# Kernel optimization log

Measured on AMD Instinct MI355X. Metric: run time of the kernel, lower is better.

## Reference

```python
import jax, jax.numpy as jnp
import numpy as np

N = 100000   # nodes in batched graph
E = 1600000  # edges (before self-loops)
D = 128      # in_dim == hidden_dim == num_outputs
G = 64       # graphs in the batch


def setup_inputs() -> dict:
    key = jax.random.key(0)
    ks = jax.random.split(key, 8)
    s = 1.0 / np.sqrt(D)
    x = jax.random.normal(ks[0], (N, D), jnp.float32)
    src = jax.random.randint(ks[1], (E,), 0, N, dtype=jnp.int64)
    dst = jax.random.randint(ks[2], (E,), 0, N, dtype=jnp.int64)
    graph_ids = jnp.sort(jax.random.randint(ks[3], (N,), 0, G, dtype=jnp.int64))
    W0 = jax.random.normal(ks[4], (D, D), jnp.float32) * s
    W1 = jax.random.normal(ks[5], (D, D), jnp.float32) * s
    W2 = jax.random.normal(ks[6], (D, D), jnp.float32) * s
    b0 = jnp.zeros((D,), jnp.float32)
    b1 = jnp.zeros((D,), jnp.float32)
    b2 = jnp.zeros((D,), jnp.float32)
    return {"x": x, "W0": W0, "b0": b0, "W1": W1, "b1": b1,
            "W2": W2, "b2": b2, "src": src, "dst": dst, "graph_ids": graph_ids}


def reference(x, W0, b0, W1, b1, W2, b2, src, dst, graph_ids):
    n = x.shape[0]
    loops = jnp.arange(n, dtype=src.dtype)
    src_f = jnp.concatenate([src, loops])  # add self-loops once (dgl.add_self_loop)
    dst_f = jnp.concatenate([dst, loops])
    ones_e = jnp.ones(src_f.shape, x.dtype)
    deg_out = jax.ops.segment_sum(ones_e, src_f, num_segments=n)  # >=1 (self-loop)
    deg_in = jax.ops.segment_sum(ones_e, dst_f, num_segments=n)
    cs = jax.lax.rsqrt(deg_out)[:, None]  # source norm (GraphConv norm='both')
    cd = jax.lax.rsqrt(deg_in)[:, None]   # destination norm

    def gcn_layer(h, W, b):
        m = (h * cs)[src_f]                                   # [E+N, D] gather
        agg = jax.ops.segment_sum(m, dst_f, num_segments=n)   # scatter-add SpMM
        return jax.nn.relu((agg * cd) @ W + b)                # F.relu(conv(g, h))

    h = gcn_layer(x, W0, b0)
    h = gcn_layer(h, W1, b1)
    h = gcn_layer(h, W2, b2)

    # dgl.mean_nodes: per-graph mean over nodes
    sums = jax.ops.segment_sum(h, graph_ids, num_segments=G)
    cnt = jax.ops.segment_sum(jnp.ones((n, 1), h.dtype), graph_ids, num_segments=G)
    return sums / jnp.maximum(cnt, 1.0)  # [G, D] logits
```

## Files before the change

### kernel.cpp

```cpp
#include <hip/hip_runtime.h>
#include <stdint.h>

#define D 128
#define CAP 64
#define HB 128
#define CH 50000

typedef __attribute__((ext_vector_type(8))) short bf16x8;
typedef __attribute__((ext_vector_type(4))) float f32x4;

__device__ inline unsigned short f2bf(float x) {
  union { float f; uint32_t u; } v; v.f = x;
  uint32_t u = v.u;
  u += 0x7fffu + ((u >> 16) & 1u);
  return (unsigned short)(u >> 16);
}
__device__ inline float bflo(uint32_t u) {
  union { uint32_t u; float f; } v; v.u = u << 16; return v.f;
}
__device__ inline float bfhi(uint32_t u) {
  union { uint32_t u; float f; } v; v.u = u & 0xffff0000u; return v.f;
}
__device__ inline uint32_t packbf(float lo, float hi) {
  return (uint32_t)f2bf(lo) | ((uint32_t)f2bf(hi) << 16);
}

__global__ __launch_bounds__(256) void hist_kernel(
    const int* __restrict__ src, const int* __restrict__ dst,
    unsigned int* __restrict__ parts_s, unsigned int* __restrict__ parts_d,
    int E, int N) {
  __shared__ unsigned int lbs[CH / 8];
  __shared__ unsigned int lbd[CH / 8];
  int b = blockIdx.x & (HB - 1);
  int lo = (blockIdx.x >> 7) * CH;
  for (int i = threadIdx.x; i < CH / 8; i += 256) { lbs[i] = 0; lbd[i] = 0; }
  __syncthreads();
  int per = (E + HB - 1) / HB;
  int e0 = b * per;
  int e1 = min(e0 + per, E);
  for (int e = e0 + threadIdx.x; e < e1; e += 256) {
    int rs = src[e] - lo;
    if ((unsigned)rs < CH) atomicAdd(&lbs[rs >> 3], 1u << ((rs & 7) * 4));
    int rd = dst[e] - lo;
    if ((unsigned)rd < CH) atomicAdd(&lbd[rd >> 3], 1u << ((rd & 7) * 4));
  }
  __syncthreads();
  int nu = (N + 7) / 8;
  int base = lo >> 3;
  int cu = min(CH / 8, nu - base);
  unsigned int* ps = parts_s + (size_t)b * nu + base;
  unsigned int* pd = parts_d + (size_t)b * nu + base;
  for (int i = threadIdx.x; i < cu; i += 256) { ps[i] = lbs[i]; pd[i] = lbd[i]; }
}

__global__ void scan_norm_kernel(const unsigned char* __restrict__ parts_s,
                                 const unsigned char* __restrict__ parts_d,
                                 unsigned char* __restrict__ offs_d,
                                 int* __restrict__ degd,
                                 float* __restrict__ cs, float* __restrict__ cd, int N) {
  int t = blockIdx.x * blockDim.x + threadIdx.x;
  int i0 = t * 2;
  if (i0 >= N) return;
  int nb = N / 2;
  int ds0 = 0, ds1 = 0, dd0 = 0, dd1 = 0;
  for (int b = 0; b < HB; b++) {
    unsigned char sv = parts_s[(size_t)b * nb + t];
    ds0 += sv & 15; ds1 += sv >> 4;
    unsigned char dv = parts_d[(size_t)b * nb + t];
    offs_d[(size_t)b * N + i0]     = (unsigned char)min(dd0, 255);
    offs_d[(size_t)b * N + i0 + 1] = (unsigned char)min(dd1, 255);
    dd0 += dv & 15; dd1 += dv >> 4;
  }
  degd[i0] = dd0;     degd[i0 + 1] = dd1;
  cs[i0] = rsqrtf((float)ds0 + 1.0f);
  cs[i0 + 1] = rsqrtf((float)ds1 + 1.0f);
  cd[i0] = rsqrtf((float)dd0 + 1.0f);
  cd[i0 + 1] = rsqrtf((float)dd1 + 1.0f);
}

__global__ __launch_bounds__(256) void fill_kernel(
    const int* __restrict__ src, const int* __restrict__ dst,
    const unsigned char* __restrict__ offs_d, int* __restrict__ col, int E, int N) {
  __shared__ unsigned int lcur[CH / 8];
  int b = blockIdx.x & (HB - 1);
  int lo = (blockIdx.x >> 7) * CH;
  for (int i = threadIdx.x; i < CH / 8; i += 256) lcur[i] = 0;
  __syncthreads();
  int per = (E + HB - 1) / HB;
  int e0 = b * per;
  int e1 = min(e0 + per, E);
  const unsigned char* offb = offs_d + (size_t)b * N;
  for (int e = e0 + threadIdx.x; e < e1; e += 256) {
    int d = dst[e];
    int rd = d - lo;
    if ((unsigned)rd < CH) {
      unsigned old = atomicAdd(&lcur[rd >> 3], 1u << ((rd & 7) * 4));
      int local = (old >> ((rd & 7) * 4)) & 0xF;
      int pos = (int)offb[d] + local;
      if (pos < CAP) col[(size_t)d * CAP + pos] = src[e];
    }
  }
}

__global__ void prep_kernel(const float* __restrict__ W0, const float* __restrict__ W1,
                            const float* __restrict__ W2, unsigned short* __restrict__ Wt,
                            const float* __restrict__ x, const float* __restrict__ cs,
                            uint32_t* __restrict__ xs, int total2,
                            float* __restrict__ cnt, int G,
                            float* __restrict__ outz, int out_total) {
  int i = blockIdx.x * blockDim.x + threadIdx.x;
  if (i < 3 * 16384) {
    int l = i >> 14, r = i & 16383;
    int n = r >> 7, k = r & 127;
    const float* W = (l == 0) ? W0 : (l == 1) ? W1 : W2;
    Wt[i] = f2bf(W[k * 128 + n]);
  }
  if (i < G) cnt[i] = 0.f;
  if (i < out_total) outz[i] = 0.f;
  if (i < total2) {
    float2 v = ((const float2*)x)[i];
    float c = cs[i >> 6];
    xs[i] = packbf(v.x * c, v.y * c);
  }
}

__global__ __launch_bounds__(512) void fused_layer_kernel(
    const uint32_t* __restrict__ hin, const unsigned short* __restrict__ Wt,
    const float* __restrict__ bias, const float* __restrict__ cd,
    const float* __restrict__ rowscale, const int* __restrict__ degd,
    const int* __restrict__ col, unsigned short* __restrict__ hout, int N) {
  __shared__ __align__(16) uint32_t At[16 * 68];

  int wv = threadIdx.x >> 6;
  int lane = threadIdx.x & 63;
  int m = lane & 15;
  int quad = lane >> 4;

  bf16x8 bfr[4];
#pragma unroll
  for (int c = 0; c < 4; c++)
    bfr[c] = *(const bf16x8*)(Wt + (size_t)(16 * wv + m) * 128 + c * 32 + quad * 8);

#pragma unroll
  for (int j = 0; j < 2; j++) {
    int w = __builtin_amdgcn_readfirstlane(blockIdx.x * 16 + wv * 2 + j);
    float accx = 0.f, accy = 0.f;
    if (w < N) {
      int n = min(degd[w], CAP);
      const int* cw = col + (size_t)w * CAP;
      const uint32_t* hl = hin + lane;
      uint32_t selfv = hl[(size_t)w * 64];
      accx = bflo(selfv); accy = bfhi(selfv);
      int i = 0;
      for (; i + 7 < n; i += 8) {
        int s0 = cw[i],     s1 = cw[i + 1], s2 = cw[i + 2], s3 = cw[i + 3];
        int s4 = cw[i + 4], s5 = cw[i + 5], s6 = cw[i + 6], s7 = cw[i + 7];
        uint32_t v0 = hl[(size_t)s0 * 64];
        uint32_t v1 = hl[(size_t)s1 * 64];
        uint32_t v2 = hl[(size_t)s2 * 64];
        uint32_t v3 = hl[(size_t)s3 * 64];
        uint32_t v4 = hl[(size_t)s4 * 64];
        uint32_t v5 = hl[(size_t)s5 * 64];
        uint32_t v6 = hl[(size_t)s6 * 64];
        uint32_t v7 = hl[(size_t)s7 * 64];
        accx += bflo(v0); accy += bfhi(v0);
        accx += bflo(v1); accy += bfhi(v1);
        accx += bflo(v2); accy += bfhi(v2);
        accx += bflo(v3); accy += bfhi(v3);
        accx += bflo(v4); accy += bfhi(v4);
        accx += bflo(v5); accy += bfhi(v5);
        accx += bflo(v6); accy += bfhi(v6);
        accx += bflo(v7); accy += bfhi(v7);
      }
      for (; i + 3 < n; i += 4) {
        int s0 = cw[i], s1 = cw[i + 1], s2 = cw[i + 2], s3 = cw[i + 3];
        uint32_t v0 = hl[(size_t)s0 * 64];
        uint32_t v1 = hl[(size_t)s1 * 64];
        uint32_t v2 = hl[(size_t)s2 * 64];
        uint32_t v3 = hl[(size_t)s3 * 64];
        accx += bflo(v0); accy += bfhi(v0);
        accx += bflo(v1); accy += bfhi(v1);
        accx += bflo(v2); accy += bfhi(v2);
        accx += bflo(v3); accy += bfhi(v3);
      }
      for (; i < n; i++) {
        uint32_t v = hl[(size_t)cw[i] * 64];
        accx += bflo(v); accy += bfhi(v);
      }
      float cdv = cd[w];
      accx *= cdv; accy *= cdv;
    }
    At[(wv * 2 + j) * 68 + lane] = packbf(accx, accy);
  }
  __syncthreads();

  const unsigned short* arow = (const unsigned short*)At + m * 136;
  f32x4 acc = f32x4{0.f, 0.f, 0.f, 0.f};
#pragma unroll
  for (int c = 0; c < 4; c++) {
    bf16x8 a = *(const bf16x8*)(arow + c * 32 + quad * 8);
    acc = __builtin_amdgcn_mfma_f32_16x16x32_bf16(a, bfr[c], acc, 0, 0, 0);
  }
  int colb = 16 * wv + m;
  float bv = bias[colb];
#pragma unroll
  for (int i = 0; i < 4; i++) {
    int r = blockIdx.x * 16 + quad * 4 + i;
    if (r < N) {
      float v = acc[i] + bv;
      v = v > 0.f ? v : 0.f;
      if (rowscale) v *= rowscale[r];
      hout[(size_t)r * D + colb] = f2bf(v);
    }
  }
}

__global__ void pool_kernel(const unsigned short* __restrict__ h, const int* __restrict__ gid,
                            float* __restrict__ outsum, float* __restrict__ cnt, int N) {
  int v0 = blockIdx.x * 64;
  if (v0 >= N) return;
  int d = threadIdx.x;
  int vend = min(v0 + 64, N);
  int cur = gid[v0];
  float acc = 0.f, c = 0.f;
  for (int v = v0; v < vend; v++) {
    int g = gid[v];
    if (g != cur) {
      atomicAdd(&outsum[cur * D + d], acc);
      if (d == 0) atomicAdd(&cnt[cur], c);
      acc = 0.f; c = 0.f; cur = g;
    }
    unsigned short hv = __builtin_nontemporal_load(&h[(size_t)v * D + d]);
    union { uint32_t u; float f; } cv; cv.u = (uint32_t)hv << 16;
    acc += cv.f;
    c += 1.f;
  }
  atomicAdd(&outsum[cur * D + d], acc);
  if (d == 0) atomicAdd(&cnt[cur], c);
}

__global__ void div_kernel(float* out, const float* __restrict__ cnt, int total) {
  int i = blockIdx.x * blockDim.x + threadIdx.x;
  if (i < total) out[i] /= fmaxf(cnt[i >> 7], 1.0f);
}

extern "C" void kernel_launch(void* const* d_in, const int* in_sizes, int n_in,
                              void* d_out, int out_size, void* d_ws, size_t ws_size,
                              hipStream_t stream) {
  const float* x  = (const float*)d_in[0];
  const float* W0 = (const float*)d_in[1];
  const float* b0 = (const float*)d_in[2];
  const float* W1 = (const float*)d_in[3];
  const float* b1 = (const float*)d_in[4];
  const float* W2 = (const float*)d_in[5];
  const float* b2 = (const float*)d_in[6];
  const int* src  = (const int*)d_in[7];
  const int* dst  = (const int*)d_in[8];
  const int* gid  = (const int*)d_in[9];

  const int N = in_sizes[0] / D;
  const int E = in_sizes[7];
  const int G = out_size / D;
  const int nu = (N + 7) / 8;

  uint32_t* hsA = (uint32_t*)d_ws;
  uint32_t* hsB = hsA + (size_t)N * 64;
  int* col      = (int*)(hsB + (size_t)N * 64);
  int* degd     = col + (size_t)N * CAP;
  float* csb    = (float*)(degd + N);
  float* cdb    = csb + N;
  float* cnt    = cdb + N;
  unsigned short* Wt = (unsigned short*)(cnt + G);
  unsigned int* parts_s = (unsigned int*)(Wt + 3 * 16384);
  unsigned int* parts_d = parts_s + (size_t)HB * nu;
  unsigned char* offs_d = (unsigned char*)(parts_d + (size_t)HB * nu);

  const int nch = (N + CH - 1) / CH;
  hist_kernel<<<HB * nch, 256, 0, stream>>>(src, dst, parts_s, parts_d, E, N);
  scan_norm_kernel<<<(N / 2 + 255) / 256, 256, 0, stream>>>(
      (const unsigned char*)parts_s, (const unsigned char*)parts_d, offs_d,
      degd, csb, cdb, N);
  fill_kernel<<<HB * nch, 256, 0, stream>>>(src, dst, offs_d, col, E, N);
  prep_kernel<<<(N * 64 + 255) / 256, 256, 0, stream>>>(
      W0, W1, W2, Wt, x, csb, hsA, N * 64, cnt, G, (float*)d_out, out_size);

  const int ltiles = (N + 15) / 16;

  fused_layer_kernel<<<ltiles, 512, 0, stream>>>(hsA, Wt, b0, cdb, csb, degd, col,
                                                 (unsigned short*)hsB, N);
  fused_layer_kernel<<<ltiles, 512, 0, stream>>>(hsB, Wt + 16384, b1, cdb, csb, degd, col,
                                                 (unsigned short*)hsA, N);
  fused_layer_kernel<<<ltiles, 512, 0, stream>>>(hsA, Wt + 2 * 16384, b2, cdb, nullptr, degd, col,
                                                 (unsigned short*)hsB, N);

  pool_kernel<<<(N + 63) / 64, 128, 0, stream>>>((const unsigned short*)hsB, gid,
                                                 (float*)d_out, cnt, N);
  div_kernel<<<(out_size + 255) / 256, 256, 0, stream>>>((float*)d_out, cnt, out_size);
}
```

Baseline: 460.6 us.

## Fold prep work into hist/fill kernels, halve chunk size, use 4-wave layer blocks

Result: slower. 473.1 us (+2.7%).

```diff
diff --git a/kernel.cpp b/kernel.cpp
--- a/kernel.cpp
+++ b/kernel.cpp
@@ -4,7 +4,7 @@
 #define D 128
 #define CAP 64
 #define HB 128
-#define CH 50000
+#define CH 25000
 
 typedef __attribute__((ext_vector_type(8))) short bf16x8;
 typedef __attribute__((ext_vector_type(4))) float f32x4;
@@ -28,7 +28,10 @@
 __global__ __launch_bounds__(256) void hist_kernel(
     const int* __restrict__ src, const int* __restrict__ dst,
     unsigned int* __restrict__ parts_s, unsigned int* __restrict__ parts_d,
-    int E, int N) {
+    int E, int N,
+    const float* __restrict__ W0, const float* __restrict__ W1,
+    const float* __restrict__ W2, unsigned short* __restrict__ Wt,
+    float* __restrict__ cnt, int G, float* __restrict__ outz, int out_total) {
   __shared__ unsigned int lbs[CH / 8];
   __shared__ unsigned int lbd[CH / 8];
   int b = blockIdx.x & (HB - 1);
@@ -51,6 +54,16 @@
   unsigned int* ps = parts_s + (size_t)b * nu + base;
   unsigned int* pd = parts_d + (size_t)b * nu + base;
   for (int i = threadIdx.x; i < cu; i += 256) { ps[i] = lbs[i]; pd[i] = lbd[i]; }
+
+  int gs = gridDim.x * 256;
+  for (int i = blockIdx.x * 256 + threadIdx.x; i < 3 * 16384; i += gs) {
+    int l = i >> 14, r = i & 16383;
+    int n = r >> 7, k = r & 127;
+    const float* W = (l == 0) ? W0 : (l == 1) ? W1 : W2;
+    Wt[i] = f2bf(W[k * 128 + n]);
+  }
+  for (int i = blockIdx.x * 256 + threadIdx.x; i < G; i += gs) cnt[i] = 0.f;
+  for (int i = blockIdx.x * 256 + threadIdx.x; i < out_total; i += gs) outz[i] = 0.f;
 }
 
 __global__ void scan_norm_kernel(const unsigned char* __restrict__ parts_s,
@@ -80,7 +93,9 @@
 
 __global__ __launch_bounds__(256) void fill_kernel(
     const int* __restrict__ src, const int* __restrict__ dst,
-    const unsigned char* __restrict__ offs_d, int* __restrict__ col, int E, int N) {
+    const unsigned char* __restrict__ offs_d, int* __restrict__ col, int E, int N,
+    const float* __restrict__ x, const float* __restrict__ cs,
+    uint32_t* __restrict__ xs) {
   __shared__ unsigned int lcur[CH / 8];
   int b = blockIdx.x & (HB - 1);
   int lo = (blockIdx.x >> 7) * CH;
@@ -100,31 +115,16 @@
       if (pos < CAP) col[(size_t)d * CAP + pos] = src[e];
     }
   }
-}
-
-__global__ void prep_kernel(const float* __restrict__ W0, const float* __restrict__ W1,
-                            const float* __restrict__ W2, unsigned short* __restrict__ Wt,
-                            const float* __restrict__ x, const float* __restrict__ cs,
-                            uint32_t* __restrict__ xs, int total2,
-                            float* __restrict__ cnt, int G,
-                            float* __restrict__ outz, int out_total) {
-  int i = blockIdx.x * blockDim.x + threadIdx.x;
-  if (i < 3 * 16384) {
-    int l = i >> 14, r = i & 16383;
-    int n = r >> 7, k = r & 127;
-    const float* W = (l == 0) ? W0 : (l == 1) ? W1 : W2;
-    Wt[i] = f2bf(W[k * 128 + n]);
-  }
-  if (i < G) cnt[i] = 0.f;
-  if (i < out_total) outz[i] = 0.f;
-  if (i < total2) {
+  int total2 = N * 64;
+  int gs = gridDim.x * 256;
+  for (int i = blockIdx.x * 256 + threadIdx.x; i < total2; i += gs) {
     float2 v = ((const float2*)x)[i];
     float c = cs[i >> 6];
     xs[i] = packbf(v.x * c, v.y * c);
   }
 }
 
-__global__ __launch_bounds__(512) void fused_layer_kernel(
+__global__ __launch_bounds__(256) void fused_layer_kernel(
     const uint32_t* __restrict__ hin, const unsigned short* __restrict__ Wt,
     const float* __restrict__ bias, const float* __restrict__ cd,
     const float* __restrict__ rowscale, const int* __restrict__ degd,
@@ -136,14 +136,17 @@
   int m = lane & 15;
   int quad = lane >> 4;
 
-  bf16x8 bfr[4];
-#pragma unroll
-  for (int c = 0; c < 4; c++)
-    bfr[c] = *(const bf16x8*)(Wt + (size_t)(16 * wv + m) * 128 + c * 32 + quad * 8);
-
-#pragma unroll
-  for (int j = 0; j < 2; j++) {
-    int w = __builtin_amdgcn_readfirstlane(blockIdx.x * 16 + wv * 2 + j);
+  bf16x8 bfr[2][4];
+#pragma unroll
+  for (int tt = 0; tt < 2; tt++) {
+    int tile = 2 * wv + tt;
+#pragma unroll
+    for (int c = 0; c < 4; c++)
+      bfr[tt][c] = *(const bf16x8*)(Wt + (size_t)(16 * tile + m) * 128 + c * 32 + quad * 8);
+  }
+
+  for (int j = 0; j < 4; j++) {
+    int w = __builtin_amdgcn_readfirstlane(blockIdx.x * 16 + wv * 4 + j);
     float accx = 0.f, accy = 0.f;
     if (w < N) {
       int n = min(degd[w], CAP);
@@ -190,27 +193,32 @@
       float cdv = cd[w];
       accx *= cdv; accy *= cdv;
     }
-    At[(wv * 2 + j) * 68 + lane] = packbf(accx, accy);
+    At[(wv * 4 + j) * 68 + lane] = packbf(accx, accy);
   }
   __syncthreads();
 
   const unsigned short* arow = (const unsigned short*)At + m * 136;
-  f32x4 acc = f32x4{0.f, 0.f, 0.f, 0.f};
-#pragma unroll
-  for (int c = 0; c < 4; c++) {
-    bf16x8 a = *(const bf16x8*)(arow + c * 32 + quad * 8);
-    acc = __builtin_amdgcn_mfma_f32_16x16x32_bf16(a, bfr[c], acc, 0, 0, 0);
-  }
-  int colb = 16 * wv + m;
-  float bv = bias[colb];
-#pragma unroll
-  for (int i = 0; i < 4; i++) {
-    int r = blockIdx.x * 16 + quad * 4 + i;
-    if (r < N) {
-      float v = acc[i] + bv;
-      v = v > 0.f ? v : 0.f;
-      if (rowscale) v *= rowscale[r];
-      hout[(size_t)r * D + colb] = f2bf(v);
+  bf16x8 afrag[4];
+#pragma unroll
+  for (int c = 0; c < 4; c++) afrag[c] = *(const bf16x8*)(arow + c * 32 + quad * 8);
+
+#pragma unroll
+  for (int tt = 0; tt < 2; tt++) {
+    f32x4 acc = f32x4{0.f, 0.f, 0.f, 0.f};
+#pragma unroll
+    for (int c = 0; c < 4; c++)
+      acc = __builtin_amdgcn_mfma_f32_16x16x32_bf16(afrag[c], bfr[tt][c], acc, 0, 0, 0);
+    int colb = 16 * (2 * wv + tt) + m;
+    float bv = bias[colb];
+#pragma unroll
+    for (int i = 0; i < 4; i++) {
+      int r = blockIdx.x * 16 + quad * 4 + i;
+      if (r < N) {
+        float v = acc[i] + bv;
+        v = v > 0.f ? v : 0.f;
+        if (rowscale) v *= rowscale[r];
+        hout[(size_t)r * D + colb] = f2bf(v);
+      }
     }
   }
 }
@@ -276,21 +284,21 @@
   unsigned char* offs_d = (unsigned char*)(parts_d + (size_t)HB * nu);
 
   const int nch = (N + CH - 1) / CH;
-  hist_kernel<<<HB * nch, 256, 0, stream>>>(src, dst, parts_s, parts_d, E, N);
+  hist_kernel<<<HB * nch, 256, 0, stream>>>(src, dst, parts_s, parts_d, E, N,
+                                            W0, W1, W2, Wt, cnt, G,
+                                            (float*)d_out, out_size);
   scan_norm_kernel<<<(N / 2 + 255) / 256, 256, 0, stream>>>(
       (const unsigned char*)parts_s, (const unsigned char*)parts_d, offs_d,
       degd, csb, cdb, N);
-  fill_kernel<<<HB * nch, 256, 0, stream>>>(src, dst, offs_d, col, E, N);
-  prep_kernel<<<(N * 64 + 255) / 256, 256, 0, stream>>>(
-      W0, W1, W2, Wt, x, csb, hsA, N * 64, cnt, G, (float*)d_out, out_size);
+  fill_kernel<<<HB * nch, 256, 0, stream>>>(src, dst, offs_d, col, E, N, x, csb, hsA);
 
   const int ltiles = (N + 15) / 16;
 
-  fused_layer_kernel<<<ltiles, 512, 0, stream>>>(hsA, Wt, b0, cdb, csb, degd, col,
+  fused_layer_kernel<<<ltiles, 256, 0, stream>>>(hsA, Wt, b0, cdb, csb, degd, col,
                                                  (unsigned short*)hsB, N);
-  fused_layer_kernel<<<ltiles, 512, 0, stream>>>(hsB, Wt + 16384, b1, cdb, csb, degd, col,
+  fused_layer_kernel<<<ltiles, 256, 0, stream>>>(hsB, Wt + 16384, b1, cdb, csb, degd, col,
                                                  (unsigned short*)hsA, N);
-  fused_layer_kernel<<<ltiles, 512, 0, stream>>>(hsA, Wt + 2 * 16384, b2, cdb, nullptr, degd, col,
+  fused_layer_kernel<<<ltiles, 256, 0, stream>>>(hsA, Wt + 2 * 16384, b2, cdb, nullptr, degd, col,
                                                  (unsigned short*)hsB, N);
 
   pool_kernel<<<(N + 63) / 64, 128, 0, stream>>>((const unsigned short*)hsB, gid,
```
